# Kernel optimization log

Measured on AMD Instinct MI355X. Metric: run time of the kernel, lower is better.

## Reference

```python
import jax, jax.numpy as jnp
import numpy as np

B, N = 4, 8192
MODEL_DIM, FEAT, HEADS, DIM, SIZE = 512, 64, 8, 3, 32
BN_EPS = 1e-5


def setup_inputs() -> dict:
    key = jax.random.key(0)
    ks = jax.random.split(key, 8)
    return {
        "input": jax.random.normal(ks[0], (B, MODEL_DIM, N), jnp.float32),
        "orig_pcd": jax.random.uniform(ks[1], (B, 3, N), jnp.float32, minval=-1.0, maxval=1.0),
        "conv_w": jax.random.normal(ks[2], (HEADS * (FEAT + 3), MODEL_DIM), jnp.float32) * (MODEL_DIM ** -0.5),
        "key_gamma": jax.random.normal(ks[3], (HEADS * 3,), jnp.float32) * 0.1,
        "key_beta": jnp.zeros((HEADS * 3,), jnp.float32),
        "val_gamma": jnp.ones((HEADS * FEAT,), jnp.float32),
        "val_beta": jnp.zeros((HEADS * FEAT,), jnp.float32),
        "proj": jax.random.normal(ks[4], (HEADS, DIM, 3), jnp.float32) * 0.5,
    }


def _bn(x, gamma, beta):
    # train-mode BatchNorm1d: normalize each channel over (batch, length); x: [B, C, N]
    mu = jnp.mean(x, axis=(0, 2), keepdims=True)
    var = jnp.var(x, axis=(0, 2), keepdims=True)
    xhat = (x - mu) * jax.lax.rsqrt(var + BN_EPS)
    return xhat * gamma[None, :, None] + beta[None, :, None]


def _splat(lattice, values):
    # lattice: [B, H, DIM, N] in (-1, 1); values: [B, H*FEAT, N]
    # DifferentiablePositions: map (-1,1) -> continuous grid coords in [0, SIZE-1]
    c = (lattice + 1.0) * 0.5 * (SIZE - 1)
    f = jnp.clip(jnp.floor(c), 0, SIZE - 2).astype(jnp.int32)   # base corner
    r = c - f.astype(c.dtype)                                    # local coord, [B,H,DIM,N]
    vals = values.reshape(B, HEADS, FEAT, N)
    data = jnp.moveaxis(vals, 2, -1)                             # [B,H,N,FEAT]
    strides = jnp.array([SIZE ** (DIM - 1 - d) for d in range(DIM)], jnp.int32)
    ncells = SIZE ** DIM
    bh = jnp.arange(B)[:, None] * HEADS + jnp.arange(HEADS)[None, :]  # [B,H]
    z = jnp.zeros((B * HEADS * ncells, FEAT), jnp.float32)
    # trilinear splat: scatter-add into the 2^DIM surrounding lattice cells
    for corner in range(2 ** DIM):
        bits = jnp.array([(corner >> (DIM - 1 - d)) & 1 for d in range(DIM)], jnp.int32)
        bits4 = bits[None, None, :, None]
        idx = f + bits4                                           # [B,H,DIM,N]
        w = jnp.prod(jnp.where(bits4 == 1, r, 1.0 - r), axis=2)   # [B,H,N]
        flat = jnp.sum(idx * strides[None, None, :, None], axis=2)  # [B,H,N]
        gid = (bh[:, :, None] * ncells + flat).reshape(-1)        # [B*H*N]
        z = z.at[gid].add((data * w[..., None]).reshape(-1, FEAT))
    return z.reshape(B, HEADS, ncells, FEAT).transpose(0, 1, 3, 2).reshape((B, HEADS, FEAT) + (SIZE,) * DIM)


def reference(input, orig_pcd, conv_w, key_gamma, key_beta, val_gamma, val_beta, proj):
    # 1x1 conv == channel GEMM: [B, H*(FEAT+3), N]
    kv = jnp.einsum('om,bmn->bon', conv_w, input)
    keys_res = _bn(kv[:, :HEADS * 3], key_gamma, key_beta)        # [B, H*3, N]
    values = _bn(kv[:, HEADS * 3:], val_gamma, val_beta)          # [B, H*FEAT, N]
    # per-head learned 3D->DIM projection of (pcd + predicted offset)
    pts = orig_pcd[:, None] + keys_res.reshape(B, HEADS, 3, N)    # [B,H,3,N]
    keys = jnp.einsum('hdk,bhkn->bhdn', proj, pts)                # [B,H,DIM,N]
    lattice = jnp.tanh(keys)
    z = _splat(lattice, values)                                   # [B,H,FEAT,S,S,S]
    occ = (jnp.abs(z) > 1e-9).sum().astype(jnp.float32) / (B * FEAT * HEADS)
    return z, occ, jnp.mean(keys), jnp.var(keys)
```

## Files before the change

kernel.cpp:

```cpp
#include <hip/hip_runtime.h>

#define B_     4
#define N_     8192
#define MD_    512
#define OC_    536
#define HEADS_ 8
#define FEAT_  64
#define NC_    32768
#define ZTOT_  67108864ll
#define NPTS_  262144
#define NKEYS_ 786432.0f
#define BNINV_ (1.0f / 32768.0f)

typedef __bf16 bf16x8 __attribute__((ext_vector_type(8)));
typedef float  f32x4  __attribute__((ext_vector_type(4)));

__device__ __forceinline__ unsigned short f2bf(float f) {
  unsigned int u = __float_as_uint(f);
  u = (u + 0x7FFFu + ((u >> 16) & 1u)) >> 16;
  return (unsigned short)u;
}
__device__ __forceinline__ float bf2f(unsigned short s) {
  return __uint_as_float(((unsigned)s) << 16);
}

__global__ __launch_bounds__(256) void convw_kernel(const float* __restrict__ W,
                                                    unsigned short* __restrict__ Wbf) {
  int i = (blockIdx.x * 256 + threadIdx.x) * 4;
  float4 v = *(const float4*)&W[24 * 512 + i];
  ushort4 o;
  o.x = f2bf(v.x); o.y = f2bf(v.y); o.z = f2bf(v.z); o.w = f2bf(v.w);
  *(ushort4*)&Wbf[i] = o;
}

__global__ __launch_bounds__(256) void convxt_kernel(const float* __restrict__ X,
                                                     unsigned short* __restrict__ Xt) {
  const int n0 = blockIdx.x * 64;
  const int k0 = blockIdx.y * 64;
  const int b  = blockIdx.z;
  __shared__ float T[64][65];
  const int t = threadIdx.x;
#pragma unroll
  for (int i = 0; i < 16; ++i) {
    int idx = t + i * 256;
    int kk = idx >> 6, nn = idx & 63;
    T[kk][nn] = X[((size_t)b * MD_ + k0 + kk) * N_ + n0 + nn];
  }
  __syncthreads();
  const int sub = t & 7;
  const int nb  = t >> 3;
#pragma unroll
  for (int i = 0; i < 2; ++i) {
    int nn = nb + i * 32;
    ushort4 o0, o1;
    o0.x = f2bf(T[sub * 8 + 0][nn]); o0.y = f2bf(T[sub * 8 + 1][nn]);
    o0.z = f2bf(T[sub * 8 + 2][nn]); o0.w = f2bf(T[sub * 8 + 3][nn]);
    o1.x = f2bf(T[sub * 8 + 4][nn]); o1.y = f2bf(T[sub * 8 + 5][nn]);
    o1.z = f2bf(T[sub * 8 + 6][nn]); o1.w = f2bf(T[sub * 8 + 7][nn]);
    unsigned short* dst = Xt + ((size_t)b * N_ + n0 + nn) * MD_ + k0 + sub * 8;
    *(ushort4*)dst = o0;
    *(ushort4*)(dst + 4) = o1;
  }
}

__global__ __launch_bounds__(256) void gemm_keys(const float* __restrict__ W,
                                                 const float* __restrict__ X,
                                                 float* __restrict__ kvk,
                                                 float* __restrict__ ssum,
                                                 float* __restrict__ s2sum) {
  const int n0 = blockIdx.x * 256;
  const int b  = blockIdx.y;
  __shared__ float Wt[32][26];
  __shared__ float In[32][260];
  const int t  = threadIdx.x;
  const int cg = t & 63;
  const int rb = (t >> 6) * 6;
  float acc[6][4];
#pragma unroll
  for (int r = 0; r < 6; ++r)
#pragma unroll
    for (int c = 0; c < 4; ++c) acc[r][c] = 0.f;
  const float* Xb = X + (size_t)b * MD_ * N_;
  for (int k0 = 0; k0 < MD_; k0 += 32) {
#pragma unroll
    for (int i = 0; i < 3; ++i) {
      int idx = t * 3 + i;
      int m = idx % 24, k = idx / 24;
      Wt[k][m] = W[(size_t)m * MD_ + k0 + k];
    }
#pragma unroll
    for (int i = 0; i < 8; ++i) {
      int slot = t + i * 256;
      int k = slot >> 6, n4 = slot & 63;
      float4 v = *(const float4*)(Xb + (size_t)(k0 + k) * N_ + n0 + n4 * 4);
      *(float4*)&In[k][n4 * 4] = v;
    }
    __syncthreads();
#pragma unroll
    for (int k = 0; k < 32; ++k) {
      float4 bv = *(const float4*)&In[k][cg * 4];
#pragma unroll
      for (int r = 0; r < 6; ++r) {
        float a = Wt[k][rb + r];
        acc[r][0] = fmaf(a, bv.x, acc[r][0]);
        acc[r][1] = fmaf(a, bv.y, acc[r][1]);
        acc[r][2] = fmaf(a, bv.z, acc[r][2]);
        acc[r][3] = fmaf(a, bv.w, acc[r][3]);
      }
    }
    __syncthreads();
  }
#pragma unroll
  for (int r = 0; r < 6; ++r) {
    float* dst = kvk + ((size_t)b * 24 + rb + r) * N_ + n0 + cg * 4;
    *(float4*)dst = *(float4*)&acc[r][0];
    float s = acc[r][0] + acc[r][1] + acc[r][2] + acc[r][3];
    float s2 = acc[r][0]*acc[r][0] + acc[r][1]*acc[r][1] +
               acc[r][2]*acc[r][2] + acc[r][3]*acc[r][3];
#pragma unroll
    for (int off = 32; off; off >>= 1) {
      s  += __shfl_down(s, off);
      s2 += __shfl_down(s2, off);
    }
    if (cg == 0) { atomicAdd(&ssum[rb + r], s); atomicAdd(&s2sum[rb + r], s2); }
  }
}

__global__ __launch_bounds__(256) void gemm_mfma(const unsigned short* __restrict__ Wbf,
                                                 const unsigned short* __restrict__ Xt,
                                                 unsigned short* __restrict__ valsbf,
                                                 float* __restrict__ ssum,
                                                 float* __restrict__ s2sum) {
  const int n0 = blockIdx.x * 128;
  const int m0 = blockIdx.y * 128;
  const int b  = blockIdx.z;
  __shared__ __align__(16) unsigned short smem[128 * 144];
#define AL(r, c) smem[(r) * 72 + (c)]
#define BL(r, c) smem[128 * 72 + (r) * 72 + (c)]
#define CS(r, c) smem[(r) * 136 + (c)]
  const int t = threadIdx.x;
  const int lane = t & 63, wave = t >> 6;
  const int wm = wave >> 1, wn = wave & 1;
  f32x4 acc[4][4];
#pragma unroll
  for (int mi = 0; mi < 4; ++mi)
#pragma unroll
    for (int ni = 0; ni < 4; ++ni)
#pragma unroll
      for (int j = 0; j < 4; ++j) acc[mi][ni][j] = 0.f;

  const unsigned short* Xb = Xt + ((size_t)b * N_ + n0) * MD_;
  for (int k0 = 0; k0 < MD_; k0 += 64) {
#pragma unroll
    for (int i = 0; i < 4; ++i) {
      int chunk = t + i * 256;
      int r = chunk >> 3, c = chunk & 7;
      *(uint4*)&AL(r, c * 8) =
          *(const uint4*)&Wbf[(size_t)(m0 + r) * MD_ + k0 + c * 8];
    }
#pragma unroll
    for (int i = 0; i < 4; ++i) {
      int chunk = t + i * 256;
      int r = chunk >> 3, c = chunk & 7;
      *(uint4*)&BL(r, c * 8) =
          *(const uint4*)&Xb[(size_t)r * MD_ + k0 + c * 8];
    }
    __syncthreads();
#pragma unroll
    for (int ks = 0; ks < 2; ++ks) {
      bf16x8 af[4], bfr[4];
#pragma unroll
      for (int mi = 0; mi < 4; ++mi)
        af[mi] = *(const bf16x8*)&AL(wm * 64 + mi * 16 + (lane & 15),
                                     ks * 32 + (lane >> 4) * 8);
#pragma unroll
      for (int ni = 0; ni < 4; ++ni)
        bfr[ni] = *(const bf16x8*)&BL(wn * 64 + ni * 16 + (lane & 15),
                                      ks * 32 + (lane >> 4) * 8);
#pragma unroll
      for (int mi = 0; mi < 4; ++mi)
#pragma unroll
        for (int ni = 0; ni < 4; ++ni)
          acc[mi][ni] = __builtin_amdgcn_mfma_f32_16x16x32_bf16(
              af[mi], bfr[ni], acc[mi][ni], 0, 0, 0);
    }
    __syncthreads();
  }
#pragma unroll
  for (int mi = 0; mi < 4; ++mi)
#pragma unroll
    for (int j = 0; j < 4; ++j) {
      float s  = acc[mi][0][j] + acc[mi][1][j] + acc[mi][2][j] + acc[mi][3][j];
      float s2 = acc[mi][0][j]*acc[mi][0][j] + acc[mi][1][j]*acc[mi][1][j] +
                 acc[mi][2][j]*acc[mi][2][j] + acc[mi][3][j]*acc[mi][3][j];
#pragma unroll
      for (int off = 1; off < 16; off <<= 1) {
        s  += __shfl_xor(s, off);
        s2 += __shfl_xor(s2, off);
      }
      if ((lane & 15) == 0) {
        int mg = m0 + wm * 64 + mi * 16 + (lane >> 4) * 4 + j;
        atomicAdd(&ssum[24 + mg], s);
        atomicAdd(&s2sum[24 + mg], s2);
      }
    }
#pragma unroll
  for (int mi = 0; mi < 4; ++mi)
#pragma unroll
    for (int ni = 0; ni < 4; ++ni) {
      int row = wm * 64 + mi * 16 + (lane >> 4) * 4;
      int col = wn * 64 + ni * 16 + (lane & 15);
#pragma unroll
      for (int j = 0; j < 4; ++j)
        CS(row + j, col) = f2bf(acc[mi][ni][j]);
    }
  __syncthreads();
#pragma unroll
  for (int i = 0; i < 4; ++i) {
    int row = (t >> 3) + i * 32;
    int cb  = (t & 7) * 16;
    uint4 lo = *(const uint4*)&CS(row, cb);
    uint4 hi = *(const uint4*)&CS(row, cb + 8);
    unsigned short* dst = valsbf + ((size_t)b * 512 + m0 + row) * N_ + n0 + cb;
    *(uint4*)dst       = lo;
    *(uint4*)(dst + 8) = hi;
  }
#undef AL
#undef BL
#undef CS
}

__global__ __launch_bounds__(256) void passk_kernel(const float* __restrict__ kvk,
                                                    const float* __restrict__ orig,
                                                    const float* __restrict__ proj,
                                                    const float* __restrict__ ssum,
                                                    const float* __restrict__ s2sum,
                                                    const float* __restrict__ kg,
                                                    const float* __restrict__ kb,
                                                    float4* __restrict__ cellr,
                                                    float* __restrict__ kacc) {
  const int p = blockIdx.x * 256 + threadIdx.x;
  const int bh = p >> 13, n = p & (N_ - 1);
  const int b = bh >> 3, h = bh & 7;
  const float* Kb = kvk + (size_t)b * 24 * N_;
  float pt[3];
#pragma unroll
  for (int k = 0; k < 3; ++k) {
    int ch = h * 3 + k;
    float mu  = ssum[ch] * BNINV_;
    float var = s2sum[ch] * BNINV_ - mu * mu;
    float sck = kg[ch] * rsqrtf(var + 1e-5f);
    float shk = kb[ch] - mu * sck;
    float kr = fmaf(Kb[(size_t)ch * N_ + n], sck, shk);
    pt[k] = orig[((size_t)b * 3 + k) * N_ + n] + kr;
  }
  float ksum = 0.f, ksq = 0.f;
  int cell = 0;
  float rr[3];
#pragma unroll
  for (int d = 0; d < 3; ++d) {
    const float* pr = proj + (h * 3 + d) * 3;
    float key = pr[0] * pt[0] + pr[1] * pt[1] + pr[2] * pt[2];
    ksum += key; ksq += key * key;
    float lat = tanhf(key);
    float c = (lat + 1.0f) * 15.5f;
    float fl = floorf(c);
    fl = fminf(fmaxf(fl, 0.0f), 30.0f);
    rr[d] = c - fl;
    cell += (int)fl * ((d == 0) ? 1024 : (d == 1) ? 32 : 1);
  }
  cellr[p] = make_float4(rr[0], rr[1], rr[2], __int_as_float(cell));
#pragma unroll
  for (int off = 32; off; off >>= 1) {
    ksum += __shfl_down(ksum, off);
    ksq  += __shfl_down(ksq, off);
  }
  if ((threadIdx.x & 63) == 0) {
    atomicAdd(&kacc[0], ksum);
    atomicAdd(&kacc[1], ksq);
  }
}

__global__ __launch_bounds__(1024, 1) void sortk_kernel(const float4* __restrict__ cellr,
                                                        float4* __restrict__ sorted) {
  const int bh = blockIdx.x;
  __shared__ int hist[NC_];
  __shared__ int wsum[16];
  const int t = threadIdx.x;
  for (int i = t; i < NC_; i += 1024) hist[i] = 0;
  __syncthreads();
  const float4* cr = cellr + (size_t)bh * N_;
#pragma unroll
  for (int i = 0; i < 8; ++i) {
    int cell = __float_as_int(cr[t + i * 1024].w);
    atomicAdd(&hist[cell], 1);
  }
  __syncthreads();
  const int base = t * 32;
  int s = 0;
#pragma unroll
  for (int j = 0; j < 32; ++j) s += hist[base + ((j + t) & 31)];
  const int lane = t & 63, wv = t >> 6;
  int sc = s;
#pragma unroll
  for (int off = 1; off < 64; off <<= 1) {
    int x = __shfl_up(sc, off);
    if (lane >= off) sc += x;
  }
  if (lane == 63) wsum[wv] = sc;
  __syncthreads();
  if (t < 16) {
    int x = wsum[t];
    int sc2 = x;
#pragma unroll
    for (int off = 1; off < 16; off <<= 1) {
      int y = __shfl_up(sc2, off);
      if (t >= off) sc2 += y;
    }
    wsum[t] = sc2 - x;
  }
  __syncthreads();
  int run = sc - s + wsum[wv];
#pragma unroll
  for (int j = 0; j < 32; ++j) {
    int idx = base + ((j + t) & 31);
    int v = hist[idx];
    hist[idx] = run;
    run += v;
  }
  __syncthreads();
  float4* dst = sorted + (size_t)bh * N_;
#pragma unroll
  for (int i = 0; i < 8; ++i) {
    int n = t + i * 1024;
    float4 m = cr[n];
    int cell = __float_as_int(m.w);
    int pos = atomicAdd(&hist[cell], 1);
    m.w = __int_as_float(cell | (n << 15));
    dst[pos] = m;
  }
}

__global__ __launch_bounds__(512, 1) void accum_kernel(const unsigned short* __restrict__ valsbf,
                                                       const float* __restrict__ ssum,
                                                       const float* __restrict__ s2sum,
                                                       const float* __restrict__ vg,
                                                       const float* __restrict__ vb,
                                                       const float4* __restrict__ sorted,
                                                       float* __restrict__ zout,
                                                       unsigned int* __restrict__ occ) {
  const int blk = blockIdx.x;
  const int f   = blk & 63;
  const int bh  = blk >> 6;
  const int b = bh >> 3, h = bh & 7;
  __shared__ float tile[NC_];
  const int t = threadIdx.x;
#pragma unroll
  for (int i = 0; i < 16; ++i)
    ((float4*)tile)[t + i * 512] = make_float4(0.f, 0.f, 0.f, 0.f);
  __syncthreads();

  const int ch = 24 + h * 64 + f;
  const float mu  = ssum[ch] * BNINV_;
  const float var = s2sum[ch] * BNINV_ - mu * mu;
  const float sc  = vg[ch - 24] * rsqrtf(var + 1e-5f);
  const float sh  = vb[ch - 24] - mu * sc;
  const unsigned short* kvrow = valsbf + ((size_t)b * 512 + h * 64 + f) * N_;
  const float4* sp = sorted + (size_t)bh * N_;
  const int base = t * 16;

  float4 e[16];
#pragma unroll
  for (int i = 0; i < 16; ++i) e[i] = sp[base + i];
  unsigned short kvv[16];
#pragma unroll
  for (int i = 0; i < 16; ++i)
    kvv[i] = kvrow[((unsigned)__float_as_int(e[i].w)) >> 15];

#define FLUSH8()                                                    \
  {                                                                 \
    atomicAdd(&tile[cur],        m0_);                              \
    atomicAdd(&tile[cur + 1],    m1_);                              \
    atomicAdd(&tile[cur + 32],   m2_);                              \
    atomicAdd(&tile[cur + 33],   m3_);                              \
    atomicAdd(&tile[cur + 1024], m4_);                              \
    atomicAdd(&tile[cur + 1025], m5_);                              \
    atomicAdd(&tile[cur + 1056], m6_);                              \
    atomicAdd(&tile[cur + 1057], m7_);                              \
  }

  float m0_ = 0.f, m1_ = 0.f, m2_ = 0.f, m3_ = 0.f;
  float m4_ = 0.f, m5_ = 0.f, m6_ = 0.f, m7_ = 0.f;
  int cur = __float_as_int(e[0].w) & 32767;
#pragma unroll
  for (int i = 0; i < 16; ++i) {
    int cell = __float_as_int(e[i].w) & 32767;
    if (cell != cur) {
      if (cell == cur + 1) {
        atomicAdd(&tile[cur],        m0_);
        atomicAdd(&tile[cur + 32],   m2_);
        atomicAdd(&tile[cur + 1024], m4_);
        atomicAdd(&tile[cur + 1056], m6_);
        m0_ = m1_; m2_ = m3_; m4_ = m5_; m6_ = m7_;
        m1_ = 0.f; m3_ = 0.f; m5_ = 0.f; m7_ = 0.f;
      } else {
        FLUSH8();
        m0_ = m1_ = m2_ = m3_ = m4_ = m5_ = m6_ = m7_ = 0.f;
      }
      cur = cell;
    }
    float v  = fmaf(bf2f(kvv[i]), sc, sh);
    float r0 = e[i].x, r1 = e[i].y, r2 = e[i].z;
    float va = v * (1.f - r0), vb2 = v * r0;
    float c00 = (1.f - r1) * (1.f - r2), c01 = (1.f - r1) * r2;
    float c10 = r1 * (1.f - r2),         c11 = r1 * r2;
    m0_ = fmaf(va, c00, m0_); m1_ = fmaf(va, c01, m1_);
    m2_ = fmaf(va, c10, m2_); m3_ = fmaf(va, c11, m3_);
    m4_ = fmaf(vb2, c00, m4_); m5_ = fmaf(vb2, c01, m5_);
    m6_ = fmaf(vb2, c10, m6_); m7_ = fmaf(vb2, c11, m7_);
  }
  FLUSH8();
#undef FLUSH8
  __syncthreads();

  unsigned int cnt = 0;
  float* dst = zout + (size_t)blk * NC_;
#pragma unroll
  for (int i = 0; i < 16; ++i) {
    float4 v = ((const float4*)tile)[t + i * 512];
    cnt += (fabsf(v.x) > 1e-9f) ? 1u : 0u;
    cnt += (fabsf(v.y) > 1e-9f) ? 1u : 0u;
    cnt += (fabsf(v.z) > 1e-9f) ? 1u : 0u;
    cnt += (fabsf(v.w) > 1e-9f) ? 1u : 0u;
    ((float4*)dst)[t + i * 512] = v;
  }
#pragma unroll
  for (int off = 32; off; off >>= 1) cnt += __shfl_down(cnt, off);
  __shared__ unsigned int wc[8];
  if ((t & 63) == 0) wc[t >> 6] = cnt;
  __syncthreads();
  if (t == 0) {
    unsigned int s = 0;
#pragma unroll
    for (int i = 0; i < 8; ++i) s += wc[i];
    atomicAdd(occ, s);
  }
}

__global__ __launch_bounds__(256) void gemm_full_kernel(const float* __restrict__ W,
                                                        const float* __restrict__ X,
                                                        float* __restrict__ KV) {
  const int n0 = blockIdx.x * 256;
  const int m0 = blockIdx.y * 64;
  const int b  = blockIdx.z;
  __shared__ float Wt[32][68];
  __shared__ float In[32][260];
  const int t  = threadIdx.x;
  const int tx = t & 31;
  const int ty = t >> 5;
  float acc[8][8];
#pragma unroll
  for (int r = 0; r < 8; ++r)
#pragma unroll
    for (int c = 0; c < 8; ++c) acc[r][c] = 0.f;
  const float* Xb = X + (size_t)b * MD_ * N_;
  for (int k0 = 0; k0 < MD_; k0 += 32) {
#pragma unroll
    for (int i = 0; i < 8; ++i) {
      int idx = t + i * 256;
      int m = idx >> 5, k = idx & 31;
      int mm = m0 + m;
      Wt[k][m] = (mm < OC_) ? W[(size_t)mm * MD_ + (k0 + k)] : 0.f;
    }
#pragma unroll
    for (int i = 0; i < 8; ++i) {
      int slot = t + i * 256;
      int k = slot >> 6, n4 = slot & 63;
      float4 v = *(const float4*)(Xb + (size_t)(k0 + k) * N_ + n0 + n4 * 4);
      *(float4*)&In[k][n4 * 4] = v;
    }
    __syncthreads();
#pragma unroll
    for (int k = 0; k < 32; ++k) {
      float a[8], bb[8];
      *(float4*)&a[0]  = *(const float4*)&Wt[k][ty * 8];
      *(float4*)&a[4]  = *(const float4*)&Wt[k][ty * 8 + 4];
      *(float4*)&bb[0] = *(const float4*)&In[k][tx * 4];
      *(float4*)&bb[4] = *(const float4*)&In[k][128 + tx * 4];
#pragma unroll
      for (int r = 0; r < 8; ++r)
#pragma unroll
        for (int c = 0; c < 8; ++c)
          acc[r][c] = fmaf(a[r], bb[c], acc[r][c]);
    }
    __syncthreads();
  }
#pragma unroll
  for (int r = 0; r < 8; ++r) {
    int mm = m0 + ty * 8 + r;
    if (mm < OC_) {
      float* dst = KV + ((size_t)b * OC_ + mm) * N_ + n0;
      *(float4*)(dst + tx * 4)       = *(float4*)&acc[r][0];
      *(float4*)(dst + 128 + tx * 4) = *(float4*)&acc[r][4];
    }
  }
}

__global__ __launch_bounds__(256) void bn_kernel(const float* __restrict__ KV,
                                                 const float* __restrict__ kg,
                                                 const float* __restrict__ kb,
                                                 const float* __restrict__ vg,
                                                 const float* __restrict__ vb,
                                                 float* __restrict__ scale,
                                                 float* __restrict__ shift) {
  const int o = blockIdx.x;
  const int t = threadIdx.x;
  float s = 0.f, s2 = 0.f;
  for (int idx = t; idx < B_ * N_; idx += 256) {
    int bb = idx >> 13, n = idx & (N_ - 1);
    float v = KV[((size_t)bb * OC_ + o) * N_ + n];
    s += v; s2 = fmaf(v, v, s2);
  }
#pragma unroll
  for (int off = 32; off; off >>= 1) {
    s  += __shfl_down(s, off);
    s2 += __shfl_down(s2, off);
  }
  __shared__ float rs[4], rs2[4];
  if ((t & 63) == 0) { rs[t >> 6] = s; rs2[t >> 6] = s2; }
  __syncthreads();
  if (t == 0) {
    s  = rs[0] + rs[1] + rs[2] + rs[3];
    s2 = rs2[0] + rs2[1] + rs2[2] + rs2[3];
    const float inv = 1.0f / (B_ * N_);
    float mu  = s * inv;
    float var = s2 * inv - mu * mu;
    float g, be;
    if (o < 24) { g = kg[o]; be = kb[o]; }
    else        { g = vg[o - 24]; be = vb[o - 24]; }
    float sc = g * rsqrtf(var + 1e-5f);
    scale[o] = sc;
    shift[o] = be - mu * sc;
  }
}

__global__ __launch_bounds__(256) void splat_final_kernel(const float* __restrict__ KV,
                                                          const float* __restrict__ orig,
                                                          const float* __restrict__ proj,
                                                          const float* __restrict__ scale,
                                                          const float* __restrict__ shift,
                                                          float* __restrict__ Z,
                                                          float* __restrict__ kacc) {
  const int bh = blockIdx.x >> 7;
  const int n0 = (blockIdx.x & 127) << 6;
  const int b = bh >> 3, h = bh & 7;
  __shared__ float vals[64][65];
  __shared__ int   cellS[64];
  __shared__ float rS[64][4];
  const int t = threadIdx.x;
  const float* KVb = KV + (size_t)b * OC_ * N_;
  const int ch0 = 24 + h * 64;
#pragma unroll
  for (int i = 0; i < 16; ++i) {
    int idx = t + i * 256;
    int f = idx >> 6, p = idx & 63;
    int ch = ch0 + f;
    vals[f][p] = fmaf(KVb[(size_t)ch * N_ + n0 + p], scale[ch], shift[ch]);
  }
  if (t < 64) {
    const int n = n0 + t;
    float pt[3];
#pragma unroll
    for (int k = 0; k < 3; ++k) {
      int ch = h * 3 + k;
      float kr = fmaf(KVb[(size_t)ch * N_ + n], scale[ch], shift[ch]);
      pt[k] = orig[((size_t)b * 3 + k) * N_ + n] + kr;
    }
    float ksum = 0.f, ksq = 0.f;
    int cell = 0;
    float rr[3];
#pragma unroll
    for (int d = 0; d < 3; ++d) {
      const float* pr = proj + (h * 3 + d) * 3;
      float key = pr[0] * pt[0] + pr[1] * pt[1] + pr[2] * pt[2];
      ksum += key; ksq += key * key;
      float lat = tanhf(key);
      float c = (lat + 1.0f) * 15.5f;
      float fl = floorf(c);
      fl = fminf(fmaxf(fl, 0.0f), 30.0f);
      rr[d] = c - fl;
      cell += (int)fl * ((d == 0) ? 1024 : (d == 1) ? 32 : 1);
    }
    cellS[t] = cell;
    rS[t][0] = rr[0]; rS[t][1] = rr[1]; rS[t][2] = rr[2];
#pragma unroll
    for (int off = 32; off; off >>= 1) {
      ksum += __shfl_down(ksum, off);
      ksq  += __shfl_down(ksq, off);
    }
    if (t == 0) { atomicAdd(&kacc[0], ksum); atomicAdd(&kacc[1], ksq); }
  }
  __syncthreads();
  const int w = t >> 6, l = t & 63;
  for (int pi = 0; pi < 16; ++pi) {
    int p = w * 16 + pi;
    int cell = cellS[p];
    float r0 = rS[p][0], r1 = rS[p][1], r2 = rS[p][2];
    float u0 = 1.f - r0, u1 = 1.f - r1, u2 = 1.f - r2;
    float v = vals[l][p];
#pragma unroll
    for (int c = 0; c < 8; ++c) {
      float wt = ((c & 4) ? r0 : u0) * ((c & 2) ? r1 : u1) * ((c & 1) ? r2 : u2);
      int cc = cell + ((c & 4) ? 1024 : 0) + ((c & 2) ? 32 : 0) + (c & 1);
      atomicAdd(Z + (size_t)(bh * 64 + l) * NC_ + cc, v * wt);
    }
  }
}

__global__ __launch_bounds__(256) void count_kernel(const float* __restrict__ Z,
                                                    unsigned int* __restrict__ occ) {
  unsigned int cnt = 0;
  for (long long i = (long long)blockIdx.x * blockDim.x + threadIdx.x; i < ZTOT_;
       i += (long long)gridDim.x * blockDim.x)
    cnt += (fabsf(Z[i]) > 1e-9f) ? 1u : 0u;
#pragma unroll
  for (int off = 32; off; off >>= 1) cnt += __shfl_down(cnt, off);
  __shared__ unsigned int wc[4];
  const int t = threadIdx.x;
  if ((t & 63) == 0) wc[t >> 6] = cnt;
  __syncthreads();
  if (t == 0) atomicAdd(occ, wc[0] + wc[1] + wc[2] + wc[3]);
}

__global__ void finalize_kernel(const unsigned int* __restrict__ occ,
                                const float* __restrict__ kacc,
                                float* __restrict__ tail) {
  float mean = kacc[0] / NKEYS_;
  tail[0] = (float)(*occ) * (1.0f / 2048.0f);
  tail[1] = mean;
  tail[2] = kacc[1] / NKEYS_ - mean * mean;
}

extern "C" void kernel_launch(void* const* d_in, const int* in_sizes, int n_in,
                              void* d_out, int out_size, void* d_ws, size_t ws_size,
                              hipStream_t stream) {
  const float* X    = (const float*)d_in[0];
  const float* orig = (const float*)d_in[1];
  const float* W    = (const float*)d_in[2];
  const float* kg   = (const float*)d_in[3];
  const float* kb   = (const float*)d_in[4];
  const float* vg   = (const float*)d_in[5];
  const float* vb   = (const float*)d_in[6];
  const float* proj = (const float*)d_in[7];
  float* out = (float*)d_out;

  float* P = (float*)d_ws;
  float* ssum  = P;
  float* s2sum = P + 544;
  float* kacc  = P + 1088;
  unsigned int* occ = (unsigned int*)(P + 1090);
  float* scale = P + 1152;
  float* shift = P + 1696;
  char* wsb = (char*)d_ws;

  const size_t need = (size_t)60 << 20;
  if (ws_size >= need) {
    unsigned short* Wbf    = (unsigned short*)(wsb + 65536);
    float*          kvk    = (float*)(wsb + ((size_t)1 << 20));
    float4*         sorted = (float4*)(wsb + ((size_t)5 << 20));
    unsigned short* valsbf = (unsigned short*)(wsb + ((size_t)9 << 20));
    unsigned short* Xt = (unsigned short*)out;
    float4* cellr = (float4*)((char*)out + ((size_t)48 << 20));

    hipMemsetAsync(P, 0, 4368, stream);

    convw_kernel<<<256, 256, 0, stream>>>(W, Wbf);
    convxt_kernel<<<dim3(128, 8, 4), 256, 0, stream>>>(X, Xt);
    gemm_keys<<<dim3(32, 4), 256, 0, stream>>>(W, X, kvk, ssum, s2sum);
    gemm_mfma<<<dim3(64, 4, 4), 256, 0, stream>>>(Wbf, Xt, valsbf, ssum, s2sum);
    passk_kernel<<<NPTS_ / 256, 256, 0, stream>>>(kvk, orig, proj, ssum, s2sum,
                                                  kg, kb, cellr, kacc);
    sortk_kernel<<<32, 1024, 0, stream>>>(cellr, sorted);
    accum_kernel<<<2048, 512, 0, stream>>>(valsbf, ssum, s2sum, vg, vb,
                                           sorted, out, occ);
    finalize_kernel<<<1, 1, 0, stream>>>(occ, kacc, out + ZTOT_);
  } else {
    float* kv = (float*)(wsb + 16384);
    hipMemsetAsync(P, 0, 4368, stream);
    hipMemsetAsync(out, 0, (size_t)ZTOT_ * 4, stream);
    gemm_full_kernel<<<dim3(N_ / 256, 9, B_), 256, 0, stream>>>(W, X, kv);
    bn_kernel<<<OC_, 256, 0, stream>>>(kv, kg, kb, vg, vb, scale, shift);
    splat_final_kernel<<<B_ * HEADS_ * (N_ / 64), 256, 0, stream>>>(
        kv, orig, proj, scale, shift, out, kacc);
    count_kernel<<<2048, 256, 0, stream>>>(out, occ);
    finalize_kernel<<<1, 1, 0, stream>>>(occ, kacc, out + ZTOT_);
  }
}
```

Before: 593.2 us.

## Fuse key GEMM into MFMA kernel, merge key pass into sort, stage values in LDS

The fp32 key-channel GEMM becomes an extra blockIdx.y slice of the MFMA value GEMM launch, so it runs alongside the value tiles instead of as a separate small launch. The per-point key/lattice computation moves into the sort kernel, which removes the cellr intermediate buffer round-trip and a launch. The accumulate kernel now loads each value row into shared memory once instead of gathering it from global memory by permuted index. In exchange the sort kernel does more serial work in only 32 blocks, and the extra shared-memory array in accum may lower occupancy.

```diff
diff --git a/kernel.cpp b/kernel.cpp
--- a/kernel.cpp
+++ b/kernel.cpp
@@ -63,82 +63,81 @@
   }
 }
 
-__global__ __launch_bounds__(256) void gemm_keys(const float* __restrict__ W,
+__global__ __launch_bounds__(256) void gemm_mfma(const unsigned short* __restrict__ Wbf,
+                                                 const unsigned short* __restrict__ Xt,
+                                                 const float* __restrict__ W,
                                                  const float* __restrict__ X,
+                                                 unsigned short* __restrict__ valsbf,
                                                  float* __restrict__ kvk,
                                                  float* __restrict__ ssum,
                                                  float* __restrict__ s2sum) {
-  const int n0 = blockIdx.x * 256;
-  const int b  = blockIdx.y;
-  __shared__ float Wt[32][26];
-  __shared__ float In[32][260];
-  const int t  = threadIdx.x;
-  const int cg = t & 63;
-  const int rb = (t >> 6) * 6;
-  float acc[6][4];
-#pragma unroll
-  for (int r = 0; r < 6; ++r)
-#pragma unroll
-    for (int c = 0; c < 4; ++c) acc[r][c] = 0.f;
-  const float* Xb = X + (size_t)b * MD_ * N_;
-  for (int k0 = 0; k0 < MD_; k0 += 32) {
-#pragma unroll
-    for (int i = 0; i < 3; ++i) {
-      int idx = t * 3 + i;
-      int m = idx % 24, k = idx / 24;
-      Wt[k][m] = W[(size_t)m * MD_ + k0 + k];
-    }
-#pragma unroll
-    for (int i = 0; i < 8; ++i) {
-      int slot = t + i * 256;
-      int k = slot >> 6, n4 = slot & 63;
-      float4 v = *(const float4*)(Xb + (size_t)(k0 + k) * N_ + n0 + n4 * 4);
-      *(float4*)&In[k][n4 * 4] = v;
-    }
-    __syncthreads();
-#pragma unroll
-    for (int k = 0; k < 32; ++k) {
-      float4 bv = *(const float4*)&In[k][cg * 4];
-#pragma unroll
-      for (int r = 0; r < 6; ++r) {
-        float a = Wt[k][rb + r];
-        acc[r][0] = fmaf(a, bv.x, acc[r][0]);
-        acc[r][1] = fmaf(a, bv.y, acc[r][1]);
-        acc[r][2] = fmaf(a, bv.z, acc[r][2]);
-        acc[r][3] = fmaf(a, bv.w, acc[r][3]);
+  __shared__ __align__(16) unsigned short smem[128 * 144];
+  const int t = threadIdx.x;
+  const int b = blockIdx.z;
+
+  if (blockIdx.y == 4) {
+    const int n0 = blockIdx.x * 128;
+    float* Wt = (float*)smem;
+    float* In = (float*)smem + 32 * 26;
+    const int cg = t & 31;
+    const int rb = (t >> 5) * 3;
+    float acc[3][4];
+#pragma unroll
+    for (int r = 0; r < 3; ++r)
+#pragma unroll
+      for (int c = 0; c < 4; ++c) acc[r][c] = 0.f;
+    const float* Xb = X + (size_t)b * MD_ * N_;
+    for (int k0 = 0; k0 < MD_; k0 += 32) {
+#pragma unroll
+      for (int i = 0; i < 3; ++i) {
+        int idx = t * 3 + i;
+        int m = idx % 24, k = idx / 24;
+        Wt[k * 26 + m] = W[(size_t)m * MD_ + k0 + k];
       }
-    }
-    __syncthreads();
-  }
-#pragma unroll
-  for (int r = 0; r < 6; ++r) {
-    float* dst = kvk + ((size_t)b * 24 + rb + r) * N_ + n0 + cg * 4;
-    *(float4*)dst = *(float4*)&acc[r][0];
-    float s = acc[r][0] + acc[r][1] + acc[r][2] + acc[r][3];
-    float s2 = acc[r][0]*acc[r][0] + acc[r][1]*acc[r][1] +
-               acc[r][2]*acc[r][2] + acc[r][3]*acc[r][3];
-#pragma unroll
-    for (int off = 32; off; off >>= 1) {
-      s  += __shfl_down(s, off);
-      s2 += __shfl_down(s2, off);
-    }
-    if (cg == 0) { atomicAdd(&ssum[rb + r], s); atomicAdd(&s2sum[rb + r], s2); }
-  }
-}
-
-__global__ __launch_bounds__(256) void gemm_mfma(const unsigned short* __restrict__ Wbf,
-                                                 const unsigned short* __restrict__ Xt,
-                                                 unsigned short* __restrict__ valsbf,
-                                                 float* __restrict__ ssum,
-                                                 float* __restrict__ s2sum) {
-  const int n0 = blockIdx.x * 128;
-  const int m0 = blockIdx.y * 128;
-  const int b  = blockIdx.z;
-  __shared__ __align__(16) unsigned short smem[128 * 144];
+#pragma unroll
+      for (int i = 0; i < 4; ++i) {
+        int slot = t + i * 256;
+        int k = slot >> 5, n4 = slot & 31;
+        float4 v = *(const float4*)(Xb + (size_t)(k0 + k) * N_ + n0 + n4 * 4);
+        *(float4*)&In[k * 132 + n4 * 4] = v;
+      }
+      __syncthreads();
+#pragma unroll
+      for (int k = 0; k < 32; ++k) {
+        float4 bv = *(const float4*)&In[k * 132 + cg * 4];
+#pragma unroll
+        for (int r = 0; r < 3; ++r) {
+          float a = Wt[k * 26 + rb + r];
+          acc[r][0] = fmaf(a, bv.x, acc[r][0]);
+          acc[r][1] = fmaf(a, bv.y, acc[r][1]);
+          acc[r][2] = fmaf(a, bv.z, acc[r][2]);
+          acc[r][3] = fmaf(a, bv.w, acc[r][3]);
+        }
+      }
+      __syncthreads();
+    }
+#pragma unroll
+    for (int r = 0; r < 3; ++r) {
+      float* dst = kvk + ((size_t)b * 24 + rb + r) * N_ + n0 + cg * 4;
+      *(float4*)dst = *(float4*)&acc[r][0];
+      float s = acc[r][0] + acc[r][1] + acc[r][2] + acc[r][3];
+      float s2 = acc[r][0]*acc[r][0] + acc[r][1]*acc[r][1] +
+                 acc[r][2]*acc[r][2] + acc[r][3]*acc[r][3];
+#pragma unroll
+      for (int off = 16; off; off >>= 1) {
+        s  += __shfl_down(s, off, 32);
+        s2 += __shfl_down(s2, off, 32);
+      }
+      if (cg == 0) { atomicAdd(&ssum[rb + r], s); atomicAdd(&s2sum[rb + r], s2); }
+    }
+    return;
+  }
+
 #define AL(r, c) smem[(r) * 72 + (c)]
 #define BL(r, c) smem[128 * 72 + (r) * 72 + (c)]
 #define CS(r, c) smem[(r) * 136 + (c)]
-  const int t = threadIdx.x;
+  const int n0 = blockIdx.x * 128;
+  const int m0 = blockIdx.y * 128;
   const int lane = t & 63, wave = t >> 6;
   const int wm = wave >> 1, wn = wave & 1;
   f32x4 acc[4][4];
@@ -230,72 +229,74 @@
 #undef CS
 }
 
-__global__ __launch_bounds__(256) void passk_kernel(const float* __restrict__ kvk,
-                                                    const float* __restrict__ orig,
-                                                    const float* __restrict__ proj,
-                                                    const float* __restrict__ ssum,
-                                                    const float* __restrict__ s2sum,
-                                                    const float* __restrict__ kg,
-                                                    const float* __restrict__ kb,
-                                                    float4* __restrict__ cellr,
-                                                    float* __restrict__ kacc) {
-  const int p = blockIdx.x * 256 + threadIdx.x;
-  const int bh = p >> 13, n = p & (N_ - 1);
+__global__ __launch_bounds__(1024, 1) void sortk_kernel(const float* __restrict__ kvk,
+                                                        const float* __restrict__ orig,
+                                                        const float* __restrict__ proj,
+                                                        const float* __restrict__ ssum,
+                                                        const float* __restrict__ s2sum,
+                                                        const float* __restrict__ kg,
+                                                        const float* __restrict__ kb,
+                                                        float4* __restrict__ sorted,
+                                                        float* __restrict__ kacc) {
+  const int bh = blockIdx.x;
   const int b = bh >> 3, h = bh & 7;
-  const float* Kb = kvk + (size_t)b * 24 * N_;
-  float pt[3];
+  __shared__ int hist[NC_];
+  __shared__ int wsum[16];
+  const int t = threadIdx.x;
+  for (int i = t; i < NC_; i += 1024) hist[i] = 0;
+
+  float sck[3], shk[3];
 #pragma unroll
   for (int k = 0; k < 3; ++k) {
     int ch = h * 3 + k;
     float mu  = ssum[ch] * BNINV_;
     float var = s2sum[ch] * BNINV_ - mu * mu;
-    float sck = kg[ch] * rsqrtf(var + 1e-5f);
-    float shk = kb[ch] - mu * sck;
-    float kr = fmaf(Kb[(size_t)ch * N_ + n], sck, shk);
-    pt[k] = orig[((size_t)b * 3 + k) * N_ + n] + kr;
-  }
+    sck[k] = kg[ch] * rsqrtf(var + 1e-5f);
+    shk[k] = kb[ch] - mu * sck[k];
+  }
+  __syncthreads();
+
+  const float* Kb = kvk + (size_t)b * 24 * N_;
+  const float* Ob = orig + (size_t)b * 3 * N_;
+  float4 mreg[8];
   float ksum = 0.f, ksq = 0.f;
-  int cell = 0;
-  float rr[3];
-#pragma unroll
-  for (int d = 0; d < 3; ++d) {
-    const float* pr = proj + (h * 3 + d) * 3;
-    float key = pr[0] * pt[0] + pr[1] * pt[1] + pr[2] * pt[2];
-    ksum += key; ksq += key * key;
-    float lat = tanhf(key);
-    float c = (lat + 1.0f) * 15.5f;
-    float fl = floorf(c);
-    fl = fminf(fmaxf(fl, 0.0f), 30.0f);
-    rr[d] = c - fl;
-    cell += (int)fl * ((d == 0) ? 1024 : (d == 1) ? 32 : 1);
-  }
-  cellr[p] = make_float4(rr[0], rr[1], rr[2], __int_as_float(cell));
+#pragma unroll
+  for (int i = 0; i < 8; ++i) {
+    const int n = t + i * 1024;
+    float pt[3];
+#pragma unroll
+    for (int k = 0; k < 3; ++k) {
+      float kr = fmaf(Kb[(size_t)(h * 3 + k) * N_ + n], sck[k], shk[k]);
+      pt[k] = Ob[(size_t)k * N_ + n] + kr;
+    }
+    int cell = 0;
+    float rr[3];
+#pragma unroll
+    for (int d = 0; d < 3; ++d) {
+      const float* pr = proj + (h * 3 + d) * 3;
+      float key = pr[0] * pt[0] + pr[1] * pt[1] + pr[2] * pt[2];
+      ksum += key; ksq += key * key;
+      float lat = tanhf(key);
+      float c = (lat + 1.0f) * 15.5f;
+      float fl = floorf(c);
+      fl = fminf(fmaxf(fl, 0.0f), 30.0f);
+      rr[d] = c - fl;
+      cell += (int)fl * ((d == 0) ? 1024 : (d == 1) ? 32 : 1);
+    }
+    mreg[i] = make_float4(rr[0], rr[1], rr[2], __int_as_float(cell | (n << 15)));
+    atomicAdd(&hist[cell], 1);
+  }
 #pragma unroll
   for (int off = 32; off; off >>= 1) {
     ksum += __shfl_down(ksum, off);
     ksq  += __shfl_down(ksq, off);
   }
-  if ((threadIdx.x & 63) == 0) {
+  if ((t & 63) == 0) {
     atomicAdd(&kacc[0], ksum);
     atomicAdd(&kacc[1], ksq);
   }
-}
-
-__global__ __launch_bounds__(1024, 1) void sortk_kernel(const float4* __restrict__ cellr,
-                                                        float4* __restrict__ sorted) {
-  const int bh = blockIdx.x;
-  __shared__ int hist[NC_];
-  __shared__ int wsum[16];
-  const int t = threadIdx.x;
-  for (int i = t; i < NC_; i += 1024) hist[i] = 0;
-  __syncthreads();
-  const float4* cr = cellr + (size_t)bh * N_;
-#pragma unroll
-  for (int i = 0; i < 8; ++i) {
-    int cell = __float_as_int(cr[t + i * 1024].w);
-    atomicAdd(&hist[cell], 1);
-  }
-  __syncthreads();
+  __syncthreads();
+
   const int base = t * 32;
   int s = 0;
 #pragma unroll
@@ -332,11 +333,9 @@
   float4* dst = sorted + (size_t)bh * N_;
 #pragma unroll
   for (int i = 0; i < 8; ++i) {
-    int n = t + i * 1024;
-    float4 m = cr[n];
-    int cell = __float_as_int(m.w);
+    float4 m = mreg[i];
+    int cell = __float_as_int(m.w) & 32767;
     int pos = atomicAdd(&hist[cell], 1);
-    m.w = __int_as_float(cell | (n << 15));
     dst[pos] = m;
   }
 }
@@ -354,10 +353,14 @@
   const int bh  = blk >> 6;
   const int b = bh >> 3, h = bh & 7;
   __shared__ float tile[NC_];
+  __shared__ unsigned short kvs[N_];
   const int t = threadIdx.x;
 #pragma unroll
   for (int i = 0; i < 16; ++i)
     ((float4*)tile)[t + i * 512] = make_float4(0.f, 0.f, 0.f, 0.f);
+  const unsigned short* kvrow = valsbf + ((size_t)b * 512 + h * 64 + f) * N_;
+  ((uint4*)kvs)[t]       = ((const uint4*)kvrow)[t];
+  ((uint4*)kvs)[t + 512] = ((const uint4*)kvrow)[t + 512];
   __syncthreads();
 
   const int ch = 24 + h * 64 + f;
@@ -365,17 +368,12 @@
   const float var = s2sum[ch] * BNINV_ - mu * mu;
   const float sc  = vg[ch - 24] * rsqrtf(var + 1e-5f);
   const float sh  = vb[ch - 24] - mu * sc;
-  const unsigned short* kvrow = valsbf + ((size_t)b * 512 + h * 64 + f) * N_;
   const float4* sp = sorted + (size_t)bh * N_;
   const int base = t * 16;
 
   float4 e[16];
 #pragma unroll
   for (int i = 0; i < 16; ++i) e[i] = sp[base + i];
-  unsigned short kvv[16];
-#pragma unroll
-  for (int i = 0; i < 16; ++i)
-    kvv[i] = kvrow[((unsigned)__float_as_int(e[i].w)) >> 15];
 
 #define FLUSH8()                                                    \
   {                                                                 \
@@ -394,7 +392,8 @@
   int cur = __float_as_int(e[0].w) & 32767;
 #pragma unroll
   for (int i = 0; i < 16; ++i) {
-    int cell = __float_as_int(e[i].w) & 32767;
+    int packed = __float_as_int(e[i].w);
+    int cell = packed & 32767;
     if (cell != cur) {
       if (cell == cur + 1) {
         atomicAdd(&tile[cur],        m0_);
@@ -409,7 +408,7 @@
       }
       cur = cell;
     }
-    float v  = fmaf(bf2f(kvv[i]), sc, sh);
+    float v  = fmaf(bf2f(kvs[(unsigned)packed >> 15]), sc, sh);
     float r0 = e[i].x, r1 = e[i].y, r2 = e[i].z;
     float va = v * (1.f - r0), vb2 = v * r0;
     float c00 = (1.f - r1) * (1.f - r2), c01 = (1.f - r1) * r2;
@@ -670,17 +669,15 @@
     float4*         sorted = (float4*)(wsb + ((size_t)5 << 20));
     unsigned short* valsbf = (unsigned short*)(wsb + ((size_t)9 << 20));
     unsigned short* Xt = (unsigned short*)out;
-    float4* cellr = (float4*)((char*)out + ((size_t)48 << 20));
 
     hipMemsetAsync(P, 0, 4368, stream);
 
     convw_kernel<<<256, 256, 0, stream>>>(W, Wbf);
     convxt_kernel<<<dim3(128, 8, 4), 256, 0, stream>>>(X, Xt);
-    gemm_keys<<<dim3(32, 4), 256, 0, stream>>>(W, X, kvk, ssum, s2sum);
-    gemm_mfma<<<dim3(64, 4, 4), 256, 0, stream>>>(Wbf, Xt, valsbf, ssum, s2sum);
-    passk_kernel<<<NPTS_ / 256, 256, 0, stream>>>(kvk, orig, proj, ssum, s2sum,
-                                                  kg, kb, cellr, kacc);
-    sortk_kernel<<<32, 1024, 0, stream>>>(cellr, sorted);
+    gemm_mfma<<<dim3(64, 5, 4), 256, 0, stream>>>(Wbf, Xt, W, X,
+                                                  valsbf, kvk, ssum, s2sum);
+    sortk_kernel<<<32, 1024, 0, stream>>>(kvk, orig, proj, ssum, s2sum,
+                                          kg, kb, sorted, kacc);
     accum_kernel<<<2048, 512, 0, stream>>>(valsbf, ssum, s2sum, vg, vb,
                                            sorted, out, occ);
     finalize_kernel<<<1, 1, 0, stream>>>(occ, kacc, out + ZTOT_);
```

Result: faster. 484.0 us (median of 2 runs) (-18.4%).
